# Performance work log

Measured on AMD Instinct MI355X. Metric: run time of the kernel, lower is better.

Reference implementation:

```python
import jax, jax.numpy as jnp
import numpy as np

D = 1024
NS = 12
B = 32
S = 128
K = 512


def setup_inputs() -> dict:
    key = jax.random.key(0)
    ks = jax.random.split(key, 20)
    w = 0.02  # weight scale (xavier-ish)
    return {
        "context": jax.random.normal(ks[0], (B, S, D), jnp.float32),
        "question": jax.random.normal(ks[1], (B, 2 * D), jnp.float32),
        "knowledge": jax.random.normal(ks[2], (B, D, K), jnp.float32),
        "control_init": jax.random.normal(ks[3], (1, 1), jnp.float32),
        # position-aware linears, one per step: Linear(2d, d)
        "pa_w": jax.random.normal(ks[4], (NS, D, 2 * D), jnp.float32) * w,
        "pa_b": jnp.zeros((NS, D), jnp.float32),
        # control unit
        "cq_w": jax.random.normal(ks[5], (D, 2 * D), jnp.float32) * w,
        "cq_b": jnp.zeros((D,), jnp.float32),
        "ca_w": jax.random.normal(ks[6], (1, D), jnp.float32) * w,
        "ca_b": jnp.zeros((1,), jnp.float32),
        # read unit
        "rm_w": jax.random.normal(ks[7], (D, D), jnp.float32) * w,
        "rm_b": jnp.zeros((D,), jnp.float32),
        "ri_w": jax.random.normal(ks[8], (D, 2 * D), jnp.float32) * w,
        "ri_b": jnp.zeros((D,), jnp.float32),
        "ra_w": jax.random.normal(ks[9], (1, D), jnp.float32) * w,
        "ra_b": jnp.zeros((1,), jnp.float32),
        # write unit
        "wm_w": jax.random.normal(ks[10], (D, 2 * D), jnp.float32) * w,
        "wm_b": jnp.zeros((D,), jnp.float32),
    }


def _mac_forward(context, question, knowledge, control_init,
                 pa_w, pa_b, cq_w, cq_b, ca_w, ca_b,
                 rm_w, rm_b, ri_w, ri_b, ra_w, ra_b, wm_w, wm_b):
    b = question.shape[0]
    d = pa_w.shape[1]
    know = jnp.swapaxes(knowledge, 1, 2)  # [B, K, d]
    # all position-aware projections of the question: [n_steps, B, d]
    q_pa_all = jnp.einsum('bq,sdq->sbd', question, pa_w) + pa_b[:, None, :]
    control0 = jnp.broadcast_to(control_init, (b, d))  # randn(1,1).expand(b,d)
    memory0 = q_pa_all[0]

    def step(carry, q_pa):
        control, memory = carry
        # --- control unit ---
        cq = jnp.concatenate([control, q_pa], axis=1) @ cq_w.T + cq_b  # [B, d]
        c_att = jnp.einsum('bsd,d->bs', cq[:, None, :] * context, ca_w[0]) + ca_b[0]
        c_att = jax.nn.softmax(c_att, axis=1)
        new_control = jnp.einsum('bs,bsd->bd', c_att, context)
        # --- read unit ---
        mem_p = memory @ rm_w.T + rm_b  # [B, d]
        inter = mem_p[:, None, :] * know  # [B, K, d]
        inter = jnp.concatenate([inter, know], axis=2) @ ri_w.T + ri_b  # [B, K, d]
        r_att = jnp.einsum('bkd,d->bk', new_control[:, None, :] * inter, ra_w[0]) + ra_b[0]
        r_att = jax.nn.softmax(r_att, axis=1)
        read = jnp.einsum('bk,bkd->bd', r_att, know)
        # --- write unit ---
        new_memory = jnp.concatenate([read, memory], axis=1) @ wm_w.T + wm_b
        return (new_control, new_memory), None

    (control, memory), _ = jax.lax.scan(step, (control0, memory0), q_pa_all)
    return memory


def reference(context, question, knowledge, control_init,
              pa_w, pa_b, cq_w, cq_b, ca_w, ca_b,
              rm_w, rm_b, ri_w, ri_b, ra_w, ra_b, wm_w, wm_b):
    return _mac_forward(context, question, knowledge, control_init,
                        pa_w, pa_b, cq_w, cq_b, ca_w, ca_b,
                        rm_w, rm_b, ri_w, ri_b, ra_w, ra_b, wm_w, wm_b)
```

## Files before the change

### kernel.cpp

```cpp
#include <hip/hip_runtime.h>


#define NSTEP 12

struct GemmArgs {
  const float* X1; long x1g;
  const float* X2; long x2g;
  int c1, c2;
  const float* W; int ldw; long wg;
  const float* bias; long biasg;
  const float* addend; long addg;
  const float* xscale;
  float* out; long outg;
  int N;
};

__global__ __launch_bounds__(256) void gemm32_kernel(GemmArgs a) {
  __shared__ float xs[32 * 512];
  const int g = blockIdx.y;
  const int C = a.c1 + a.c2;
  const float* X1 = a.X1 + (long)g * a.x1g;
  const float* X2 = a.X2 ? a.X2 + (long)g * a.x2g : nullptr;
  const float* W = a.W + (long)g * a.wg;
  const int wave = threadIdx.x >> 6;
  const int lane = threadIdx.x & 63;
  const int n = blockIdx.x * 4 + wave;
  const float* wrow = W + (long)n * a.ldw;
  float acc[32];
#pragma unroll
  for (int b = 0; b < 32; b++) acc[b] = 0.f;

  for (int c0 = 0; c0 < C; c0 += 512) {
    __syncthreads();
#pragma unroll
    for (int i = 0; i < 16; i++) {
      int idx = threadIdx.x + 256 * i;
      int b = idx >> 7;
      int c4 = idx & 127;
      int c = c0 + c4 * 4;
      float4 v;
      if (c < a.c1) v = *(const float4*)(X1 + (long)b * a.c1 + c);
      else          v = *(const float4*)(X2 + (long)b * a.c2 + (c - a.c1));
      if (a.xscale) {
        float4 s = *(const float4*)(a.xscale + c);
        v.x *= s.x; v.y *= s.y; v.z *= s.z; v.w *= s.w;
      }
      *(float4*)(xs + b * 512 + c4 * 4) = v;
    }
    __syncthreads();
#pragma unroll
    for (int i = 0; i < 2; i++) {
      int c = i * 256 + lane * 4;
      float4 wv = *(const float4*)(wrow + c0 + c);
#pragma unroll
      for (int b = 0; b < 32; b++) {
        float4 xv = *(const float4*)(xs + b * 512 + c);
        acc[b] += wv.x * xv.x + wv.y * xv.y + wv.z * xv.z + wv.w * xv.w;
      }
    }
  }
  float res = 0.f;
#pragma unroll
  for (int b = 0; b < 32; b++) {
    float v = acc[b];
#pragma unroll
    for (int off = 32; off; off >>= 1) v += __shfl_xor(v, off, 64);
    if (lane == b) res = v;
  }
  if (lane < 32) {
    float o = res;
    if (a.bias) o += a.bias[(long)g * a.biasg + n];
    if (a.addend) o += a.addend[(long)g * a.addg + (long)lane * a.N + n];
    a.out[(long)g * a.outg + (long)lane * a.N + n] = o;
  }
}

__global__ __launch_bounds__(1024) void init_control_kernel(const float* ci, float* control) {
  control[blockIdx.x * 1024 + threadIdx.x] = ci[0];
}

__global__ __launch_bounds__(1024) void transpose_kernel(const float* in, float* out) {
  __shared__ float t[32][33];
  int j0 = blockIdx.x * 32;
  int d0 = blockIdx.y * 32;
  int tx = threadIdx.x, ty = threadIdx.y;
  t[ty][tx] = in[(long)(d0 + ty) * 2048 + j0 + tx];
  __syncthreads();
  out[(long)(j0 + ty) * 1024 + d0 + tx] = t[tx][ty];
}

__global__ __launch_bounds__(1024) void ctrl_att_kernel(const float* cq, const float* context,
                                                        const float* ca_w, float* control) {
  int b = blockIdx.x;
  __shared__ float u[1024];
  __shared__ float sc[128];
  int tid = threadIdx.x;
  int wave = tid >> 6, lane = tid & 63;
  u[tid] = cq[b * 1024 + tid] * ca_w[tid];
  __syncthreads();
  const float* ctx = context + (long)b * 128 * 1024;
#pragma unroll
  for (int i = 0; i < 8; i++) {
    int s = wave * 8 + i;
    float v = 0.f;
#pragma unroll
    for (int c = 0; c < 16; c++) v += u[c * 64 + lane] * ctx[(long)s * 1024 + c * 64 + lane];
#pragma unroll
    for (int off = 32; off; off >>= 1) v += __shfl_xor(v, off, 64);
    if (lane == 0) sc[s] = v;
  }
  __syncthreads();
  if (wave == 0) {
    float a0 = sc[lane], a1 = sc[lane + 64];
    float m = fmaxf(a0, a1);
#pragma unroll
    for (int off = 32; off; off >>= 1) m = fmaxf(m, __shfl_xor(m, off, 64));
    float e0 = expf(a0 - m), e1 = expf(a1 - m);
    float s2 = e0 + e1;
#pragma unroll
    for (int off = 32; off; off >>= 1) s2 += __shfl_xor(s2, off, 64);
    float inv = 1.f / s2;
    sc[lane] = e0 * inv;
    sc[lane + 64] = e1 * inv;
  }
  __syncthreads();
  float acc = 0.f;
  for (int s = 0; s < 128; s++) acc += sc[s] * ctx[(long)s * 1024 + tid];
  control[b * 1024 + tid] = acc;
}

__global__ __launch_bounds__(512) void ratt_kernel(const float* knowledge, const float* mem_p,
                                                   const float* h, float* partial) {
  int b = blockIdx.x, jc = blockIdx.y;
  int j0 = jc * 64;
  __shared__ float gl[64];
  if (threadIdx.x < 64) {
    int j = j0 + threadIdx.x;
    gl[threadIdx.x] = mem_p[b * 1024 + j] * h[b * 2048 + j] + h[b * 2048 + 1024 + j];
  }
  __syncthreads();
  int k = threadIdx.x;
  const float* kb = knowledge + ((long)b * 1024 + j0) * 512 + k;
  float acc = 0.f;
#pragma unroll 8
  for (int jj = 0; jj < 64; jj++) acc += gl[jj] * kb[(long)jj * 512];
  partial[((long)jc * 32 + b) * 512 + k] = acc;
}

__global__ __launch_bounds__(256) void read_kernel(const float* partial, const float* knowledge,
                                                   float* readv) {
  int b = blockIdx.x, dg = blockIdx.y;
  __shared__ float aw[512];
  __shared__ float red[4];
  int tid = threadIdx.x;
  int wave = tid >> 6, lane = tid & 63;
  int k0 = tid * 2;
  float r0 = 0.f, r1 = 0.f;
#pragma unroll
  for (int p = 0; p < 16; p++) {
    const float* pp = partial + ((long)p * 32 + b) * 512;
    r0 += pp[k0];
    r1 += pp[k0 + 1];
  }
  float m = fmaxf(r0, r1);
#pragma unroll
  for (int off = 32; off; off >>= 1) m = fmaxf(m, __shfl_xor(m, off, 64));
  if (lane == 0) red[wave] = m;
  __syncthreads();
  m = fmaxf(fmaxf(red[0], red[1]), fmaxf(red[2], red[3]));
  __syncthreads();
  float e0 = expf(r0 - m), e1 = expf(r1 - m);
  float s2 = e0 + e1;
#pragma unroll
  for (int off = 32; off; off >>= 1) s2 += __shfl_xor(s2, off, 64);
  if (lane == 0) red[wave] = s2;
  __syncthreads();
  s2 = red[0] + red[1] + red[2] + red[3];
  float inv = 1.f / s2;
  aw[k0] = e0 * inv;
  aw[k0 + 1] = e1 * inv;
  __syncthreads();
  int d0 = dg * 32 + wave * 8;
  float acc[8];
#pragma unroll
  for (int i = 0; i < 8; i++) acc[i] = 0.f;
  const float* kb = knowledge + ((long)b * 1024 + d0) * 512;
  for (int kc = 0; kc < 8; kc++) {
    int kk = kc * 64 + lane;
    float av = aw[kk];
#pragma unroll
    for (int dd = 0; dd < 8; dd++) acc[dd] += av * kb[(long)dd * 512 + kk];
  }
#pragma unroll
  for (int dd = 0; dd < 8; dd++) {
    float v = acc[dd];
#pragma unroll
    for (int off = 32; off; off >>= 1) v += __shfl_xor(v, off, 64);
    if (lane == dd) readv[b * 1024 + d0 + dd] = v;
  }
}

static inline void launch_gemm(const float* X1, long x1g, const float* X2, long x2g,
                               int c1, int c2, const float* W, int ldw, long wg,
                               const float* bias, long biasg,
                               const float* addend, long addg,
                               const float* xscale, float* out, long outg, int N, int G,
                               hipStream_t stream) {
  GemmArgs a{X1, x1g, X2, x2g, c1, c2, W, ldw, wg, bias, biasg, addend, addg, xscale, out, outg, N};
  gemm32_kernel<<<dim3(N / 4, G), 256, 0, stream>>>(a);
}

extern "C" void kernel_launch(void* const* d_in, const int* in_sizes, int n_in,
                              void* d_out, int out_size, void* d_ws, size_t ws_size,
                              hipStream_t stream) {
  const float* context      = (const float*)d_in[0];
  const float* question     = (const float*)d_in[1];
  const float* knowledge    = (const float*)d_in[2];
  const float* control_init = (const float*)d_in[3];
  const float* pa_w = (const float*)d_in[4];
  const float* pa_b = (const float*)d_in[5];
  const float* cq_w = (const float*)d_in[6];
  const float* cq_b = (const float*)d_in[7];
  const float* ca_w = (const float*)d_in[8];
  const float* rm_w = (const float*)d_in[10];
  const float* rm_b = (const float*)d_in[11];
  const float* ri_w = (const float*)d_in[12];
  const float* ra_w = (const float*)d_in[14];
  const float* wm_w = (const float*)d_in[16];
  const float* wm_b = (const float*)d_in[17];
  float* out = (float*)d_out;

  float* p = (float*)d_ws;
  float* q_pa_all = p; p += NSTEP * 32 * 1024;
  float* qc_all   = p; p += NSTEP * 32 * 1024;
  float* ri_wT    = p; p += 2048 * 1024;
  float* control  = p; p += 32 * 1024;
  float* mem0     = p; p += 32 * 1024;
  float* mem1     = p; p += 32 * 1024;
  float* cq       = p; p += 32 * 1024;
  float* mem_p    = p; p += 32 * 1024;
  float* h        = p; p += 32 * 2048;
  float* partial  = p; p += 16 * 32 * 512;
  float* readv    = p; p += 32 * 1024;

  init_control_kernel<<<32, 1024, 0, stream>>>(control_init, control);
  transpose_kernel<<<dim3(64, 32), dim3(32, 32), 0, stream>>>(ri_w, ri_wT);
  launch_gemm(question, 0, nullptr, 0, 2048, 0, pa_w, 2048, 1024L * 2048,
              pa_b, 1024, nullptr, 0, nullptr, q_pa_all, 32 * 1024, 1024, NSTEP, stream);
  hipMemcpyAsync(mem0, q_pa_all, 32 * 1024 * sizeof(float), hipMemcpyDeviceToDevice, stream);
  launch_gemm(q_pa_all, 32 * 1024, nullptr, 0, 1024, 0, cq_w + 1024, 2048, 0,
              nullptr, 0, nullptr, 0, nullptr, qc_all, 32 * 1024, 1024, NSTEP, stream);

  float* mems[2] = {mem0, mem1};
  for (int s = 0; s < NSTEP; s++) {
    float* mo = mems[s & 1];
    float* mn = (s == NSTEP - 1) ? out : mems[(s + 1) & 1];
    launch_gemm(control, 0, nullptr, 0, 1024, 0, cq_w, 2048, 0,
                cq_b, 0, qc_all + (long)s * 32 * 1024, 0, nullptr, cq, 0, 1024, 1, stream);
    launch_gemm(mo, 0, nullptr, 0, 1024, 0, rm_w, 1024, 0,
                rm_b, 0, nullptr, 0, nullptr, mem_p, 0, 1024, 1, stream);
    ctrl_att_kernel<<<32, 1024, 0, stream>>>(cq, context, ca_w, control);
    launch_gemm(control, 0, nullptr, 0, 1024, 0, ri_wT, 1024, 0,
                nullptr, 0, nullptr, 0, ra_w, h, 0, 2048, 1, stream);
    ratt_kernel<<<dim3(32, 16), 512, 0, stream>>>(knowledge, mem_p, h, partial);
    read_kernel<<<dim3(32, 32), 256, 0, stream>>>(partial, knowledge, readv);
    launch_gemm(readv, 0, mo, 0, 1024, 1024, wm_w, 2048, 0,
                wm_b, 0, nullptr, 0, nullptr, mn, 0, 1024, 1, stream);
  }
}
```

Measured before the change: 1.671 ms.

## Register-tile gemm32 over 4 weight rows by 16 batches with butterfly reduction

Each wave now handles 4 output columns for half of the 32 batch rows, so each shared-memory X load feeds four weight rows. The K chunk is cut from 512 to 256 floats, halving LDS use per block, and launch bounds ask for 4 blocks per SIMD. The 32 separate full-wave shuffle reductions are replaced by a recursive-halving butterfly that leaves each lane holding one finished output. This raises the 64-register accumulator pressure and doubles the number of K-chunk iterations and barriers.

```diff
diff --git a/kernel.cpp b/kernel.cpp
--- a/kernel.cpp
+++ b/kernel.cpp
@@ -15,8 +15,8 @@
   int N;
 };
 
-__global__ __launch_bounds__(256) void gemm32_kernel(GemmArgs a) {
-  __shared__ float xs[32 * 512];
+__global__ __launch_bounds__(256, 4) void gemm32_kernel(GemmArgs a) {
+  __shared__ float xs[32 * 256];
   const int g = blockIdx.y;
   const int C = a.c1 + a.c2;
   const float* X1 = a.X1 + (long)g * a.x1g;
@@ -24,19 +24,20 @@
   const float* W = a.W + (long)g * a.wg;
   const int wave = threadIdx.x >> 6;
   const int lane = threadIdx.x & 63;
-  const int n = blockIdx.x * 4 + wave;
-  const float* wrow = W + (long)n * a.ldw;
-  float acc[32];
-#pragma unroll
-  for (int b = 0; b < 32; b++) acc[b] = 0.f;
-
-  for (int c0 = 0; c0 < C; c0 += 512) {
+  const int n0 = blockIdx.x * 8 + (wave >> 1) * 4;
+  const int bh = (wave & 1) * 16;
+  const float* wrow = W + (long)n0 * a.ldw;
+  float acc[64];
+#pragma unroll
+  for (int v = 0; v < 64; v++) acc[v] = 0.f;
+
+  for (int c0 = 0; c0 < C; c0 += 256) {
     __syncthreads();
 #pragma unroll
-    for (int i = 0; i < 16; i++) {
-      int idx = threadIdx.x + 256 * i;
-      int b = idx >> 7;
-      int c4 = idx & 127;
+    for (int r = 0; r < 8; r++) {
+      int idx = threadIdx.x + 256 * r;
+      int b = idx >> 6;
+      int c4 = idx & 63;
       int c = c0 + c4 * 4;
       float4 v;
       if (c < a.c1) v = *(const float4*)(X1 + (long)b * a.c1 + c);
@@ -45,34 +46,40 @@
         float4 s = *(const float4*)(a.xscale + c);
         v.x *= s.x; v.y *= s.y; v.z *= s.z; v.w *= s.w;
       }
-      *(float4*)(xs + b * 512 + c4 * 4) = v;
+      *(float4*)(xs + b * 256 + c4 * 4) = v;
     }
     __syncthreads();
-#pragma unroll
-    for (int i = 0; i < 2; i++) {
-      int c = i * 256 + lane * 4;
-      float4 wv = *(const float4*)(wrow + c0 + c);
-#pragma unroll
-      for (int b = 0; b < 32; b++) {
-        float4 xv = *(const float4*)(xs + b * 512 + c);
-        acc[b] += wv.x * xv.x + wv.y * xv.y + wv.z * xv.z + wv.w * xv.w;
-      }
+    const int c = lane * 4;
+    const float* wp = wrow + c0 + c;
+    float4 wv0 = *(const float4*)(wp);
+    float4 wv1 = *(const float4*)(wp + (long)a.ldw);
+    float4 wv2 = *(const float4*)(wp + 2 * (long)a.ldw);
+    float4 wv3 = *(const float4*)(wp + 3 * (long)a.ldw);
+#pragma unroll
+    for (int b = 0; b < 16; b++) {
+      float4 xv = *(const float4*)(xs + (bh + b) * 256 + c);
+      acc[b * 4 + 0] += wv0.x * xv.x + wv0.y * xv.y + wv0.z * xv.z + wv0.w * xv.w;
+      acc[b * 4 + 1] += wv1.x * xv.x + wv1.y * xv.y + wv1.z * xv.z + wv1.w * xv.w;
+      acc[b * 4 + 2] += wv2.x * xv.x + wv2.y * xv.y + wv2.z * xv.z + wv2.w * xv.w;
+      acc[b * 4 + 3] += wv3.x * xv.x + wv3.y * xv.y + wv3.z * xv.z + wv3.w * xv.w;
     }
   }
-  float res = 0.f;
-#pragma unroll
-  for (int b = 0; b < 32; b++) {
-    float v = acc[b];
-#pragma unroll
-    for (int off = 32; off; off >>= 1) v += __shfl_xor(v, off, 64);
-    if (lane == b) res = v;
-  }
-  if (lane < 32) {
-    float o = res;
-    if (a.bias) o += a.bias[(long)g * a.biasg + n];
-    if (a.addend) o += a.addend[(long)g * a.addg + (long)lane * a.N + n];
-    a.out[(long)g * a.outg + (long)lane * a.N + n] = o;
-  }
+#pragma unroll
+  for (int o = 32; o; o >>= 1) {
+    bool up = (lane & o) != 0;
+#pragma unroll
+    for (int i = 0; i < o; i++) {
+      float keep = up ? acc[i + o] : acc[i];
+      float send = up ? acc[i] : acc[i + o];
+      acc[i] = keep + __shfl_xor(send, o, 64);
+    }
+  }
+  const int bo = bh + (lane >> 2);
+  const int nn = n0 + (lane & 3);
+  float res = acc[0];
+  if (a.bias) res += a.bias[(long)g * a.biasg + nn];
+  if (a.addend) res += a.addend[(long)g * a.addg + (long)bo * a.N + nn];
+  a.out[(long)g * a.outg + (long)bo * a.N + nn] = res;
 }
 
 __global__ __launch_bounds__(1024) void init_control_kernel(const float* ci, float* control) {
@@ -207,7 +214,7 @@
                                const float* xscale, float* out, long outg, int N, int G,
                                hipStream_t stream) {
   GemmArgs a{X1, x1g, X2, x2g, c1, c2, W, ldw, wg, bias, biasg, addend, addg, xscale, out, outg, N};
-  gemm32_kernel<<<dim3(N / 4, G), 256, 0, stream>>>(a);
+  gemm32_kernel<<<dim3(N / 8, G), 256, 0, stream>>>(a);
 }
 
 extern "C" void kernel_launch(void* const* d_in, const int* in_sizes, int n_in,
```

Result: slower. 2.179 ms (+30.4%).
